# Performance work log

Measured on AMD Instinct MI355X. Metric: run time of the kernel, lower is better.

Reference implementation:

```python
import jax, jax.numpy as jnp
import numpy as np

N = 100000       # nodes
E = 1600000      # edges (avg degree 16)
D_IN = 128
D_H = 128
N_CLS = 100      # = 25 * timesteps (timesteps=4)


def setup_inputs() -> dict:
    key = jax.random.key(0)
    ks = jax.random.split(key, 16)
    x = jax.random.normal(ks[0], (N, D_IN), dtype=jnp.float32)
    edge_index = jax.random.randint(ks[1], (2, E), 0, N, dtype=jnp.int64)

    def lin_w(k, fan_in, fan_out):
        return (jax.random.normal(k, (fan_in, fan_out), dtype=jnp.float32)
                / np.float32(np.sqrt(fan_in)))

    return {
        "x": x, "edge_index": edge_index,
        "W1": lin_w(ks[2], D_IN, D_H),  "b1": jnp.zeros((D_H,), jnp.float32),
        "W2": lin_w(ks[3], D_H, D_H),   "b2": jnp.zeros((D_H,), jnp.float32),
        "W3": lin_w(ks[4], D_H, D_H),   "b3": jnp.zeros((D_H,), jnp.float32),
        "W4": lin_w(ks[5], D_H, D_H),   "b4": jnp.zeros((D_H,), jnp.float32),
        "W5": lin_w(ks[6], D_H, N_CLS), "b5": jnp.zeros((N_CLS,), jnp.float32),
        "Wl": lin_w(ks[7], N_CLS, N_CLS), "bl": jnp.zeros((N_CLS,), jnp.float32),
    }


def _gcn_conv(x, W, b, src, dst, dinv):
    # PyG GCNConv: out = D^{-1/2} (A + I) D^{-1/2} (x W) + b
    h = x @ W                                        # [N, F_out]
    msg = h[src] * (dinv[src] * dinv[dst])[:, None]  # per-edge messages [E, F_out]
    agg = jax.ops.segment_sum(msg, dst, num_segments=N)
    agg = agg + h * (dinv * dinv)[:, None]           # self-loop term
    return agg + b


def reference(x, edge_index, W1, b1, W2, b2, W3, b3, W4, b4, W5, b5, Wl, bl):
    src, dst = edge_index[0], edge_index[1]
    # degrees including self-loop (edge weight 1)
    deg = jax.ops.segment_sum(jnp.ones((E,), x.dtype), dst, num_segments=N) + 1.0
    dinv = jax.lax.rsqrt(deg)

    h = jax.nn.relu(_gcn_conv(x, W1, b1, src, dst, dinv))
    h = _gcn_conv(h, W2, b2, src, dst, dinv)
    h = _gcn_conv(h, W3, b3, src, dst, dinv)
    h = _gcn_conv(h, W4, b4, src, dst, dinv)
    h = _gcn_conv(h, W5, b5, src, dst, dinv)
    # view(N, -1) is identity here ([N, N_CLS])
    return h @ Wl + bl
```

## Files before the change

### kernel.cpp

```cpp
#include <hip/hip_runtime.h>


typedef _Float16 h16;
typedef _Float16 __attribute__((ext_vector_type(4))) h16x4;
typedef _Float16 __attribute__((ext_vector_type(8))) h16x8;
typedef float __attribute__((ext_vector_type(4))) f32x4;

static __device__ __forceinline__ float f4get(const float4& v, int k) {
  switch (k) { case 0: return v.x; case 1: return v.y; case 2: return v.z; default: return v.w; }
}

__global__ void k_detect(const int* __restrict__ edge, int* __restrict__ flag) {
  int t = threadIdx.x;
  if (edge[2 * t + 1] != 0) atomicOr(flag, 1);
}

static __device__ __forceinline__ int load_idx(const int* edge, const int* flag, size_t pos) {
  bool is64 = (*flag == 0);
  if (is64) return (int)((const long long*)edge)[pos];
  return edge[pos];
}

__global__ void k_count(const int* __restrict__ edge, const int* __restrict__ flag,
                        int* __restrict__ counts, int* __restrict__ rank,
                        int* __restrict__ dstc, int E) {
  int i = blockIdx.x * 256 + threadIdx.x;
  if (i >= E) return;
  int d = load_idx(edge, flag, (size_t)E + i);
  dstc[i] = d;
  rank[i] = atomicAdd(&counts[d], 1);
}

__global__ void k_dinv(const int* __restrict__ counts, float* __restrict__ dinv, int n) {
  int i = blockIdx.x * 256 + threadIdx.x;
  if (i < n) dinv[i] = rsqrtf((float)counts[i] + 1.0f);
}

__global__ void k_chunksum(const int* __restrict__ counts, int* __restrict__ chunksums, int n) {
  __shared__ int sd[256];
  int t = threadIdx.x;
  int base = blockIdx.x * 1024 + t * 4;
  int s = 0;
#pragma unroll
  for (int j = 0; j < 4; ++j) { int i = base + j; if (i < n) s += counts[i]; }
  sd[t] = s; __syncthreads();
  for (int off = 128; off > 0; off >>= 1) {
    if (t < off) sd[t] += sd[t + off];
    __syncthreads();
  }
  if (t == 0) chunksums[blockIdx.x] = sd[0];
}

__global__ void k_root(const int* __restrict__ chunksums, int* __restrict__ chunkbase, int nchunks) {
  __shared__ int sc[128];
  int t = threadIdx.x;
  int v = (t < nchunks) ? chunksums[t] : 0;
  sc[t] = v; __syncthreads();
  for (int off = 1; off < 128; off <<= 1) {
    int x = (t >= off) ? sc[t - off] : 0;
    __syncthreads();
    sc[t] += x;
    __syncthreads();
  }
  if (t < nchunks) chunkbase[t] = sc[t] - v;
}

__global__ void k_scan3(const int* __restrict__ counts, const int* __restrict__ chunkbase,
                        int* __restrict__ offsets, int n, int E) {
  __shared__ int sd[256];
  int t = threadIdx.x;
  int base = blockIdx.x * 1024 + t * 4;
  int c[4]; int s = 0;
#pragma unroll
  for (int j = 0; j < 4; ++j) { int i = base + j; c[j] = (i < n) ? counts[i] : 0; s += c[j]; }
  sd[t] = s; __syncthreads();
  int v = s;
  for (int off = 1; off < 256; off <<= 1) {
    int x = (t >= off) ? sd[t - off] : 0;
    __syncthreads();
    sd[t] += x;
    __syncthreads();
  }
  int run = chunkbase[blockIdx.x] + sd[t] - v;
#pragma unroll
  for (int j = 0; j < 4; ++j) {
    int i = base + j;
    if (i < n) offsets[i] = run;
    run += c[j];
  }
  if (blockIdx.x == 0 && t == 0) offsets[n] = E;
}

__global__ void k_fill(const int* __restrict__ edge, const int* __restrict__ flag,
                       const int* __restrict__ offsets, const int* __restrict__ rank,
                       const int* __restrict__ dstc, int* __restrict__ col, int E) {
  int i = blockIdx.x * 256 + threadIdx.x;
  if (i >= E) return;
  int s = load_idx(edge, flag, (size_t)i);
  int d = dstc[i];
  col[offsets[d] + rank[i]] = s;
}

__global__ void k_smm(const float* __restrict__ A, const float* __restrict__ B,
                      float* __restrict__ C, int M, int K, int Nc) {
  int idx = blockIdx.x * 256 + threadIdx.x;
  if (idx >= M * Nc) return;
  int i = idx / Nc, j = idx % Nc;
  float acc = 0.f;
  for (int k = 0; k < K; ++k) acc = fmaf(A[i * K + k], B[k * Nc + j], acc);
  C[idx] = acc;
}

__global__ void k_cvec(const float* __restrict__ b2, const float* __restrict__ b3,
                       const float* __restrict__ b4, const float* __restrict__ b5,
                       const float* __restrict__ bl, const float* __restrict__ Wl,
                       const float* __restrict__ R3, const float* __restrict__ R4,
                       const float* __restrict__ R5, float* __restrict__ corr) {
  int j = threadIdx.x;
  if (j >= 100) return;
  float a2 = 0.f, a3 = 0.f, a4 = 0.f, acb = 0.f;
  for (int k = 0; k < 128; ++k) {
    a2 = fmaf(b2[k], R3[k * 100 + j], a2);
    a3 = fmaf(b3[k], R4[k * 100 + j], a3);
    a4 = fmaf(b4[k], R5[k * 100 + j], a4);
  }
  for (int k = 0; k < 100; ++k) acb = fmaf(b5[k], Wl[k * 100 + j], acb);
  corr[j] = a2; corr[128 + j] = a3; corr[256 + j] = a4; corr[384 + j] = acb + bl[j];
}

template <typename TX, int K, int M, int OS, int AUG>
__launch_bounds__(256)
__global__ void k_mm(const TX* __restrict__ X, const float* __restrict__ W,
                     const float* __restrict__ dinv, h16* __restrict__ out, int n) {
  __shared__ float Xs[128 * 36];
  __shared__ float Ws[32 * 132];
  int tid = threadIdx.x;
  int row0 = blockIdx.x * 128;
  int tc = tid & 15, tr = tid >> 4;
  int c0 = tc * 8;
  float acc[8][8];
#pragma unroll
  for (int i = 0; i < 8; ++i)
#pragma unroll
    for (int j = 0; j < 8; ++j) acc[i][j] = 0.f;

  for (int kc = 0; kc < K; kc += 32) {
    __syncthreads();
    for (int idx = tid * 4; idx < 32 * 128; idx += 1024) {
      int r = idx >> 7, c = idx & 127;
      float4 v = make_float4(0.f, 0.f, 0.f, 0.f);
      if (c < M) v = *(const float4*)&W[(size_t)(kc + r) * M + c];
      *(float4*)&Ws[r * 132 + c] = v;
    }
    if (sizeof(TX) == 4) {
      for (int idx = tid * 4; idx < 128 * 32; idx += 1024) {
        int r = idx >> 5, c = idx & 31;
        f32x4 v = {0.f, 0.f, 0.f, 0.f};
        if (row0 + r < n)
          v = __builtin_nontemporal_load(
              (const f32x4*)&((const float*)X)[(size_t)(row0 + r) * K + kc + c]);
        *(f32x4*)&Xs[r * 36 + c] = v;
      }
    } else {
      for (int idx = tid * 8; idx < 128 * 32; idx += 2048) {
        int r = idx >> 5, c = idx & 31;
        float f[8];
#pragma unroll
        for (int q = 0; q < 8; ++q) f[q] = 0.f;
        if (row0 + r < n) {
          const h16* p = &((const h16*)X)[(size_t)(row0 + r) * K + kc + c];
          h16x8 v8 = __builtin_nontemporal_load((const h16x8*)p);
#pragma unroll
          for (int q = 0; q < 8; ++q) f[q] = (float)v8[q];
        }
        *(float4*)&Xs[r * 36 + c]     = make_float4(f[0], f[1], f[2], f[3]);
        *(float4*)&Xs[r * 36 + c + 4] = make_float4(f[4], f[5], f[6], f[7]);
      }
    }
    __syncthreads();

    for (int k = 0; k < 32; k += 4) {
      float4 xf[8];
#pragma unroll
      for (int i = 0; i < 8; ++i) xf[i] = *(const float4*)&Xs[(tr + 16 * i) * 36 + k];
      float4 wa[4], wb[4];
#pragma unroll
      for (int kk = 0; kk < 4; ++kk) {
        wa[kk] = *(const float4*)&Ws[(k + kk) * 132 + c0];
        wb[kk] = *(const float4*)&Ws[(k + kk) * 132 + c0 + 4];
      }
#pragma unroll
      for (int i = 0; i < 8; ++i) {
#pragma unroll
        for (int kk = 0; kk < 4; ++kk) {
          float xv = f4get(xf[i], kk);
          acc[i][0] = fmaf(xv, wa[kk].x, acc[i][0]);
          acc[i][1] = fmaf(xv, wa[kk].y, acc[i][1]);
          acc[i][2] = fmaf(xv, wa[kk].z, acc[i][2]);
          acc[i][3] = fmaf(xv, wa[kk].w, acc[i][3]);
          acc[i][4] = fmaf(xv, wb[kk].x, acc[i][4]);
          acc[i][5] = fmaf(xv, wb[kk].y, acc[i][5]);
          acc[i][6] = fmaf(xv, wb[kk].z, acc[i][6]);
          acc[i][7] = fmaf(xv, wb[kk].w, acc[i][7]);
        }
      }
    }
  }

#pragma unroll
  for (int i = 0; i < 8; ++i) {
    int grow = row0 + tr + 16 * i;
    if (grow >= n) continue;
    if (c0 >= OS) continue;
    float sc = dinv[grow];
    h16x8 pk;
#pragma unroll
    for (int j = 0; j < 8; ++j) {
      int colj = c0 + j;
      float vv = (colj < M) ? acc[i][j] * sc : ((AUG && colj == 100) ? sc : 0.f);
      pk[j] = (h16)vv;
    }
    *(h16x8*)&out[(size_t)grow * OS + c0] = pk;
  }
}

template <int WIDTH, int MODE>
__global__ void k_agg(const h16* __restrict__ hs, const int* __restrict__ offsets,
                      const int* __restrict__ col, const float* __restrict__ dinv,
                      const float* __restrict__ bias, const float* __restrict__ corr,
                      void* __restrict__ out, int n, int fresh) {
  const int STRIDE = 128;
  int gw = (blockIdx.x * 256 + threadIdx.x) >> 6;
  int lane = threadIdx.x & 63;
  int half = lane >> 5, sl = lane & 31;
  int v = gw * 2 + half;
  int c = sl * 4;
  if (v >= n) return;
  if (c >= WIDTH) return;
  const h16* row = &hs[(size_t)v * STRIDE];
  h16x4 selfv = *(const h16x4*)&row[c];
  float a0 = (float)selfv[0], a1 = (float)selfv[1];
  float a2 = (float)selfv[2], a3 = (float)selfv[3];
  int s = offsets[v], e = offsets[v + 1];
  for (int i = s; i < e; i += 16) {
    h16x4 m[16];
#pragma unroll
    for (int j = 0; j < 16; ++j) {
      h16x4 z = {(h16)0.f, (h16)0.f, (h16)0.f, (h16)0.f};
      m[j] = z;
      if (i + j < e) {
        int u = col[i + j];
        m[j] = *(const h16x4*)&hs[(size_t)u * STRIDE + c];
      }
    }
#pragma unroll
    for (int j = 0; j < 16; ++j) {
      a0 += (float)m[j][0]; a1 += (float)m[j][1];
      a2 += (float)m[j][2]; a3 += (float)m[j][3];
    }
  }
  float w = dinv[v];
  if (MODE == 0) {
    float r0 = fmaxf(fmaf(a0, w, bias[c]),     0.f);
    float r1 = fmaxf(fmaf(a1, w, bias[c + 1]), 0.f);
    float r2 = fmaxf(fmaf(a2, w, bias[c + 2]), 0.f);
    float r3 = fmaxf(fmaf(a3, w, bias[c + 3]), 0.f);
    h16x4 p = {(h16)r0, (h16)r1, (h16)r2, (h16)r3};
    *(h16x4*)&((h16*)out)[(size_t)v * STRIDE + c] = p;
  } else if (MODE == 1) {
    float w2 = w * w;
    float r0 = a0 * w2, r1 = a1 * w2, r2 = a2 * w2, r3 = a3 * w2;
    if (c == fresh) r0 = w;
    else if (c + 1 == fresh) r1 = w;
    else if (c + 2 == fresh) r2 = w;
    else if (c + 3 == fresh) r3 = w;
    h16x4 p = {(h16)r0, (h16)r1, (h16)r2, (h16)r3};
    *(h16x4*)&((h16*)out)[(size_t)v * STRIDE + c] = p;
  } else {
    float inv_w = 1.0f / w;
    float v3 = (float)row[100] * inv_w;
    float v2 = (float)row[101] * inv_w;
    float v1 = (float)row[102] * inv_w;
    float r[4] = {a0, a1, a2, a3};
    float4 o;
    float* op = &o.x;
#pragma unroll
    for (int q = 0; q < 4; ++q) {
      op[q] = r[q] * w + v3 * corr[c + q] + v2 * corr[128 + c + q]
            + v1 * corr[256 + c + q] + corr[384 + c + q];
    }
    *(float4*)&((float*)out)[(size_t)v * 100 + c] = o;
  }
}

extern "C" void kernel_launch(void* const* d_in, const int* in_sizes, int n_in,
                              void* d_out, int out_size, void* d_ws, size_t ws_size,
                              hipStream_t stream) {
  const float* x    = (const float*)d_in[0];
  const int*   edge = (const int*)d_in[1];
  const float* W1 = (const float*)d_in[2];  const float* b1 = (const float*)d_in[3];
  const float* W2 = (const float*)d_in[4];  const float* b2 = (const float*)d_in[5];
  const float* W3 = (const float*)d_in[6];  const float* b3 = (const float*)d_in[7];
  const float* W4 = (const float*)d_in[8];  const float* b4 = (const float*)d_in[9];
  const float* W5 = (const float*)d_in[10]; const float* b5 = (const float*)d_in[11];
  const float* Wl = (const float*)d_in[12]; const float* bl = (const float*)d_in[13];

  const int N = in_sizes[0] / 128;
  const int E = in_sizes[1] / 2;

  char* ws = (char*)d_ws;
  size_t cur = 0;
  auto alloc = [&](size_t bytes) -> char* {
    char* p = ws + cur;
    cur = (cur + bytes + 255) & ~(size_t)255;
    return p;
  };
  int*    counts    = (int*)alloc((size_t)N * 4);
  int*    flag      = (int*)alloc(4);
  int*    offsets   = (int*)alloc((size_t)(N + 1) * 4);
  float*  dinv      = (float*)alloc((size_t)N * 4);
  int*    chunksums = (int*)alloc(128 * 4);
  int*    chunkbase = (int*)alloc(128 * 4);
  float*  R5        = (float*)alloc(128 * 100 * 4);
  float*  R4        = (float*)alloc(128 * 100 * 4);
  float*  R3        = (float*)alloc(128 * 100 * 4);
  float*  Wc        = (float*)alloc(128 * 100 * 4);
  float*  corr      = (float*)alloc(512 * 4);
  int*    rank      = (int*)alloc((size_t)E * 4);
  int*    dstc      = (int*)alloc((size_t)E * 4);
  int*    col       = (int*)alloc(((size_t)E + 16) * 4);
  h16*    bufA      = (h16*)alloc((size_t)N * 128 * 2);
  h16*    bufB      = (h16*)alloc((size_t)N * 128 * 2);
  (void)ws_size; (void)n_in; (void)out_size;

  hipMemsetAsync(counts, 0, (size_t)N * 4, stream);
  hipMemsetAsync(flag, 0, 4, stream);

  const int nchunks = (N + 1023) / 1024;
  const int egrid = (E + 255) / 256;
  const int ngrid = (N + 255) / 256;

  k_detect<<<1, 256, 0, stream>>>(edge, flag);
  k_count<<<egrid, 256, 0, stream>>>(edge, flag, counts, rank, dstc, E);
  k_dinv<<<ngrid, 256, 0, stream>>>(counts, dinv, N);
  k_chunksum<<<nchunks, 256, 0, stream>>>(counts, chunksums, N);
  k_root<<<1, 128, 0, stream>>>(chunksums, chunkbase, nchunks);
  k_scan3<<<nchunks, 256, 0, stream>>>(counts, chunkbase, offsets, N, E);
  k_fill<<<egrid, 256, 0, stream>>>(edge, flag, offsets, rank, dstc, col, E);

  const int sgrid = (128 * 100 + 255) / 256;
  k_smm<<<sgrid, 256, 0, stream>>>(W5, Wl, R5, 128, 100, 100);
  k_smm<<<sgrid, 256, 0, stream>>>(W4, R5, R4, 128, 128, 100);
  k_smm<<<sgrid, 256, 0, stream>>>(W3, R4, R3, 128, 128, 100);
  k_smm<<<sgrid, 256, 0, stream>>>(W2, R3, Wc, 128, 128, 100);
  k_cvec<<<1, 128, 0, stream>>>(b2, b3, b4, b5, bl, Wl, R3, R4, R5, corr);

  const int mmgrid = (N + 127) / 128;
  const int agrid = (N + 7) / 8;

  k_mm<float, 128, 128, 128, 0><<<mmgrid, 256, 0, stream>>>(x, W1, dinv, bufA, N);
  k_agg<128, 0><<<agrid, 256, 0, stream>>>(bufA, offsets, col, dinv, b1, nullptr, bufB, N, 0);
  k_mm<h16, 128, 100, 128, 1><<<mmgrid, 256, 0, stream>>>(bufB, Wc, dinv, bufA, N);
  k_agg<104, 1><<<agrid, 256, 0, stream>>>(bufA, offsets, col, dinv, nullptr, nullptr, bufB, N, 101);
  k_agg<104, 1><<<agrid, 256, 0, stream>>>(bufB, offsets, col, dinv, nullptr, nullptr, bufA, N, 102);
  k_agg<104, 1><<<agrid, 256, 0, stream>>>(bufA, offsets, col, dinv, nullptr, nullptr, bufB, N, -1);
  k_agg<100, 2><<<agrid, 256, 0, stream>>>(bufB, offsets, col, dinv, nullptr, corr, (float*)d_out, N, -1);
}
```

Baseline: 736.5 us.

## Switch dense transform to fp16 MFMA and fold dinv into scan kernel

The dense X·W kernel now converts tiles to fp16 in shared memory and computes with 16x16x32 f16 MFMA instructions instead of scalar fp32 FMAs. W is stored transposed in LDS to match the operand layout, and dinv for the block's rows is cached in shared memory. Separately, the k_dinv launch is removed and its rsqrt is computed inside the scan kernel. The first layer's fp32 input is rounded to fp16, which costs some precision, and the output is now written as scalar fp16 stores rather than packed vectors.

After: 693.1 us. 1.06x faster.

```diff
diff --git a/kernel.cpp b/kernel.cpp
--- a/kernel.cpp
+++ b/kernel.cpp
@@ -5,10 +5,6 @@
 typedef _Float16 __attribute__((ext_vector_type(4))) h16x4;
 typedef _Float16 __attribute__((ext_vector_type(8))) h16x8;
 typedef float __attribute__((ext_vector_type(4))) f32x4;
-
-static __device__ __forceinline__ float f4get(const float4& v, int k) {
-  switch (k) { case 0: return v.x; case 1: return v.y; case 2: return v.z; default: return v.w; }
-}
 
 __global__ void k_detect(const int* __restrict__ edge, int* __restrict__ flag) {
   int t = threadIdx.x;
@@ -31,11 +27,6 @@
   rank[i] = atomicAdd(&counts[d], 1);
 }
 
-__global__ void k_dinv(const int* __restrict__ counts, float* __restrict__ dinv, int n) {
-  int i = blockIdx.x * 256 + threadIdx.x;
-  if (i < n) dinv[i] = rsqrtf((float)counts[i] + 1.0f);
-}
-
 __global__ void k_chunksum(const int* __restrict__ counts, int* __restrict__ chunksums, int n) {
   __shared__ int sd[256];
   int t = threadIdx.x;
@@ -66,7 +57,7 @@
 }
 
 __global__ void k_scan3(const int* __restrict__ counts, const int* __restrict__ chunkbase,
-                        int* __restrict__ offsets, int n, int E) {
+                        int* __restrict__ offsets, float* __restrict__ dinv, int n, int E) {
   __shared__ int sd[256];
   int t = threadIdx.x;
   int base = blockIdx.x * 1024 + t * 4;
@@ -85,7 +76,10 @@
 #pragma unroll
   for (int j = 0; j < 4; ++j) {
     int i = base + j;
-    if (i < n) offsets[i] = run;
+    if (i < n) {
+      offsets[i] = run;
+      dinv[i] = rsqrtf((float)c[j] + 1.0f);
+    }
     run += c[j];
   }
   if (blockIdx.x == 0 && t == 0) offsets[n] = E;
@@ -128,30 +122,32 @@
   corr[j] = a2; corr[128 + j] = a3; corr[256 + j] = a4; corr[384 + j] = acb + bl[j];
 }
 
-template <typename TX, int K, int M, int OS, int AUG>
+template <typename TX, int M, int AUG>
 __launch_bounds__(256)
 __global__ void k_mm(const TX* __restrict__ X, const float* __restrict__ W,
                      const float* __restrict__ dinv, h16* __restrict__ out, int n) {
-  __shared__ float Xs[128 * 36];
-  __shared__ float Ws[32 * 132];
+  const int K = 128, OS = 128;
+  __shared__ h16 Xs[128 * 40];
+  __shared__ h16 Wt[128 * 40];
+  __shared__ float dv[128];
   int tid = threadIdx.x;
   int row0 = blockIdx.x * 128;
-  int tc = tid & 15, tr = tid >> 4;
-  int c0 = tc * 8;
-  float acc[8][8];
-#pragma unroll
-  for (int i = 0; i < 8; ++i)
-#pragma unroll
-    for (int j = 0; j < 8; ++j) acc[i][j] = 0.f;
+  int w = tid >> 6, lane = tid & 63;
+  int lhi = lane >> 4, llo = lane & 15;
+
+  if (tid < 128) dv[tid] = (row0 + tid < n) ? dinv[row0 + tid] : 0.f;
+
+  f32x4 acc[2][8];
+#pragma unroll
+  for (int fr = 0; fr < 2; ++fr)
+#pragma unroll
+    for (int fc = 0; fc < 8; ++fc) {
+      f32x4 z = {0.f, 0.f, 0.f, 0.f};
+      acc[fr][fc] = z;
+    }
 
   for (int kc = 0; kc < K; kc += 32) {
     __syncthreads();
-    for (int idx = tid * 4; idx < 32 * 128; idx += 1024) {
-      int r = idx >> 7, c = idx & 127;
-      float4 v = make_float4(0.f, 0.f, 0.f, 0.f);
-      if (c < M) v = *(const float4*)&W[(size_t)(kc + r) * M + c];
-      *(float4*)&Ws[r * 132 + c] = v;
-    }
     if (sizeof(TX) == 4) {
       for (int idx = tid * 4; idx < 128 * 32; idx += 1024) {
         int r = idx >> 5, c = idx & 31;
@@ -159,68 +155,57 @@
         if (row0 + r < n)
           v = __builtin_nontemporal_load(
               (const f32x4*)&((const float*)X)[(size_t)(row0 + r) * K + kc + c]);
-        *(f32x4*)&Xs[r * 36 + c] = v;
+        h16x4 h = {(h16)v[0], (h16)v[1], (h16)v[2], (h16)v[3]};
+        *(h16x4*)&Xs[r * 40 + c] = h;
       }
     } else {
       for (int idx = tid * 8; idx < 128 * 32; idx += 2048) {
         int r = idx >> 5, c = idx & 31;
-        float f[8];
-#pragma unroll
-        for (int q = 0; q < 8; ++q) f[q] = 0.f;
-        if (row0 + r < n) {
-          const h16* p = &((const h16*)X)[(size_t)(row0 + r) * K + kc + c];
-          h16x8 v8 = __builtin_nontemporal_load((const h16x8*)p);
-#pragma unroll
-          for (int q = 0; q < 8; ++q) f[q] = (float)v8[q];
-        }
-        *(float4*)&Xs[r * 36 + c]     = make_float4(f[0], f[1], f[2], f[3]);
-        *(float4*)&Xs[r * 36 + c + 4] = make_float4(f[4], f[5], f[6], f[7]);
+        h16x8 v = {(h16)0.f, (h16)0.f, (h16)0.f, (h16)0.f,
+                   (h16)0.f, (h16)0.f, (h16)0.f, (h16)0.f};
+        if (row0 + r < n)
+          v = __builtin_nontemporal_load(
+              (const h16x8*)&((const h16*)X)[(size_t)(row0 + r) * K + kc + c]);
+        *(h16x8*)&Xs[r * 40 + c] = v;
       }
     }
-    __syncthreads();
-
-    for (int k = 0; k < 32; k += 4) {
-      float4 xf[8];
-#pragma unroll
-      for (int i = 0; i < 8; ++i) xf[i] = *(const float4*)&Xs[(tr + 16 * i) * 36 + k];
-      float4 wa[4], wb[4];
-#pragma unroll
-      for (int kk = 0; kk < 4; ++kk) {
-        wa[kk] = *(const float4*)&Ws[(k + kk) * 132 + c0];
-        wb[kk] = *(const float4*)&Ws[(k + kk) * 132 + c0 + 4];
+    for (int idx = tid * 4; idx < 32 * 128; idx += 1024) {
+      int k = idx >> 7, nn = idx & 127;
+      float4 v = make_float4(0.f, 0.f, 0.f, 0.f);
+      if (nn < M) v = *(const float4*)&W[(size_t)(kc + k) * M + nn];
+      Wt[(nn + 0) * 40 + k] = (h16)v.x;
+      Wt[(nn + 1) * 40 + k] = (h16)v.y;
+      Wt[(nn + 2) * 40 + k] = (h16)v.z;
+      Wt[(nn + 3) * 40 + k] = (h16)v.w;
+    }
+    __syncthreads();
+
+    h16x8 af0 = *(const h16x8*)&Xs[(w * 32 + llo) * 40 + lhi * 8];
+    h16x8 af1 = *(const h16x8*)&Xs[(w * 32 + 16 + llo) * 40 + lhi * 8];
+#pragma unroll
+    for (int fc = 0; fc < 8; ++fc) {
+      h16x8 bf = *(const h16x8*)&Wt[(fc * 16 + llo) * 40 + lhi * 8];
+      acc[0][fc] = __builtin_amdgcn_mfma_f32_16x16x32_f16(af0, bf, acc[0][fc], 0, 0, 0);
+      acc[1][fc] = __builtin_amdgcn_mfma_f32_16x16x32_f16(af1, bf, acc[1][fc], 0, 0, 0);
+    }
+  }
+
+#pragma unroll
+  for (int fr = 0; fr < 2; ++fr) {
+#pragma unroll
+    for (int r = 0; r < 4; ++r) {
+      int lrow = w * 32 + fr * 16 + lhi * 4 + r;
+      int grow = row0 + lrow;
+      if (grow >= n) continue;
+      float sc = dv[lrow];
+#pragma unroll
+      for (int fc = 0; fc < 8; ++fc) {
+        int colj = fc * 16 + llo;
+        float vv = (colj < M) ? acc[fr][fc][r] * sc
+                 : ((AUG && colj == 100) ? sc : 0.f);
+        out[(size_t)grow * OS + colj] = (h16)vv;
       }
-#pragma unroll
-      for (int i = 0; i < 8; ++i) {
-#pragma unroll
-        for (int kk = 0; kk < 4; ++kk) {
-          float xv = f4get(xf[i], kk);
-          acc[i][0] = fmaf(xv, wa[kk].x, acc[i][0]);
-          acc[i][1] = fmaf(xv, wa[kk].y, acc[i][1]);
-          acc[i][2] = fmaf(xv, wa[kk].z, acc[i][2]);
-          acc[i][3] = fmaf(xv, wa[kk].w, acc[i][3]);
-          acc[i][4] = fmaf(xv, wb[kk].x, acc[i][4]);
-          acc[i][5] = fmaf(xv, wb[kk].y, acc[i][5]);
-          acc[i][6] = fmaf(xv, wb[kk].z, acc[i][6]);
-          acc[i][7] = fmaf(xv, wb[kk].w, acc[i][7]);
-        }
-      }
-    }
-  }
-
-#pragma unroll
-  for (int i = 0; i < 8; ++i) {
-    int grow = row0 + tr + 16 * i;
-    if (grow >= n) continue;
-    if (c0 >= OS) continue;
-    float sc = dinv[grow];
-    h16x8 pk;
-#pragma unroll
-    for (int j = 0; j < 8; ++j) {
-      int colj = c0 + j;
-      float vv = (colj < M) ? acc[i][j] * sc : ((AUG && colj == 100) ? sc : 0.f);
-      pk[j] = (h16)vv;
-    }
-    *(h16x8*)&out[(size_t)grow * OS + c0] = pk;
+    }
   }
 }
 
@@ -338,14 +323,12 @@
 
   const int nchunks = (N + 1023) / 1024;
   const int egrid = (E + 255) / 256;
-  const int ngrid = (N + 255) / 256;
 
   k_detect<<<1, 256, 0, stream>>>(edge, flag);
   k_count<<<egrid, 256, 0, stream>>>(edge, flag, counts, rank, dstc, E);
-  k_dinv<<<ngrid, 256, 0, stream>>>(counts, dinv, N);
   k_chunksum<<<nchunks, 256, 0, stream>>>(counts, chunksums, N);
   k_root<<<1, 128, 0, stream>>>(chunksums, chunkbase, nchunks);
-  k_scan3<<<nchunks, 256, 0, stream>>>(counts, chunkbase, offsets, N, E);
+  k_scan3<<<nchunks, 256, 0, stream>>>(counts, chunkbase, offsets, dinv, N, E);
   k_fill<<<egrid, 256, 0, stream>>>(edge, flag, offsets, rank, dstc, col, E);
 
   const int sgrid = (128 * 100 + 255) / 256;
@@ -358,9 +341,9 @@
   const int mmgrid = (N + 127) / 128;
   const int agrid = (N + 7) / 8;
 
-  k_mm<float, 128, 128, 128, 0><<<mmgrid, 256, 0, stream>>>(x, W1, dinv, bufA, N);
+  k_mm<float, 128, 0><<<mmgrid, 256, 0, stream>>>(x, W1, dinv, bufA, N);
   k_agg<128, 0><<<agrid, 256, 0, stream>>>(bufA, offsets, col, dinv, b1, nullptr, bufB, N, 0);
-  k_mm<h16, 128, 100, 128, 1><<<mmgrid, 256, 0, stream>>>(bufB, Wc, dinv, bufA, N);
+  k_mm<h16, 100, 1><<<mmgrid, 256, 0, stream>>>(bufB, Wc, dinv, bufA, N);
   k_agg<104, 1><<<agrid, 256, 0, stream>>>(bufA, offsets, col, dinv, nullptr, nullptr, bufB, N, 101);
   k_agg<104, 1><<<agrid, 256, 0, stream>>>(bufB, offsets, col, dinv, nullptr, nullptr, bufA, N, 102);
   k_agg<104, 1><<<agrid, 256, 0, stream>>>(bufA, offsets, col, dinv, nullptr, nullptr, bufB, N, -1);
```
